# Kernel tuning notes

Measured on AMD Instinct MI355X. Metric: run time of the kernel, lower is better.

Reference implementation:

```python
import jax, jax.numpy as jnp
import numpy as np

B, C, T, H, W = 16, 3, 16, 224, 224
COLOR_STRENGTH = 0.3
NOISE_STRENGTH = 0.02
DROPOUT_PROB = 0.05
HFLIP_PROB = 0.5
MAX_JITTER = 3


def setup_inputs() -> dict:
    key = jax.random.key(0)
    ks = jax.random.split(key, 7)
    return {
        "video": jax.random.uniform(ks[0], (B, C, T, H, W), dtype=jnp.float32),
        "jitter": jax.random.randint(ks[1], (B,), 0, 2 * MAX_JITTER + 1, dtype=jnp.int32),
        "b_rand": jax.random.uniform(ks[2], (B,), dtype=jnp.float32),
        "c_rand": jax.random.uniform(ks[3], (B,), dtype=jnp.float32),
        "noise": jax.random.normal(ks[4], (B, C, T, H, W), dtype=jnp.float32),
        "flip_rand": jax.random.uniform(ks[5], (B,), dtype=jnp.float32),
        "drop_rand": jax.random.uniform(ks[6], (B, T), dtype=jnp.float32),
    }


def reference(video, jitter, b_rand, c_rand, noise, flip_rand, drop_rand):
    # --- GPUTemporalJitter: per-sample roll along T by j in [-MAX_JITTER, MAX_JITTER]
    j = jitter - MAX_JITTER                         # [B] in [-3, 3]
    t_idx = (jnp.arange(T)[None, :] - j[:, None]) % T  # roll semantics: out[t] = in[t - j]
    x = jnp.take_along_axis(video, t_idx[:, None, :, None, None], axis=2)

    # --- GPURandomBrightness: per-sample multiplicative factor, clamp [0,1]
    bf = 1.0 + (b_rand - 0.5) * 2.0 * COLOR_STRENGTH   # [B]
    x = jnp.clip(x * bf[:, None, None, None, None], 0.0, 1.0)

    # --- GPURandomContrast: (x-0.5)*c + 0.5 with c clamped to [0.1, 3.0], then clamp [0,1]
    cf = jnp.clip(1.0 + (c_rand - 0.5) * 2.0 * COLOR_STRENGTH, 0.1, 3.0)
    x = jnp.clip((x - 0.5) * cf[:, None, None, None, None] + 0.5, 0.0, 1.0)

    # --- GPURandomNoise: add gaussian noise, clamp [0,1]
    x = jnp.clip(x + noise * NOISE_STRENGTH, 0.0, 1.0)

    # --- GPURandomHorizontalFlip: per-sample flip along W
    flip_mask = flip_rand < HFLIP_PROB                 # [B]
    x = jnp.where(flip_mask[:, None, None, None, None], x[..., ::-1], x)

    # --- GPURandomFrameDropout: zero out frames, guarantee >=1 kept frame per sample
    keep = drop_rand > DROPOUT_PROB                    # [B, T]
    keep = keep.at[:, 0].set(keep[:, 0] | ~keep.any(axis=1))
    x = x * keep[:, None, :, None, None].astype(x.dtype)
    return x
```

## Files before the change

kernel.cpp:

```cpp
#include <hip/hip_runtime.h>

constexpr int Bn = 16, Cn = 3, Tn = 16, Hn = 224, Wn = 224;
constexpr int PLANE = Hn * Wn;
constexpr int THREADS = 256;
constexpr int FLOATS_PER_BLOCK = THREADS * 4;
constexpr int BLOCKS_PER_PLANE = PLANE / FLOATS_PER_BLOCK;

constexpr float COLOR_STRENGTH = 0.3f;
constexpr float NOISE_STRENGTH = 0.02f;
constexpr float DROPOUT_PROB   = 0.05f;
constexpr float HFLIP_PROB     = 0.5f;
constexpr int   MAX_JITTER     = 3;

__global__ __launch_bounds__(THREADS) void aug_kernel(
    const float* __restrict__ video,
    const int*   __restrict__ jitter,
    const float* __restrict__ b_rand,
    const float* __restrict__ c_rand,
    const float* __restrict__ noise,
    const float* __restrict__ flip_rand,
    const float* __restrict__ drop_rand,
    float*       __restrict__ out)
{
    const int bct = blockIdx.y;
    const int t = bct & (Tn - 1);
    const int c = (bct >> 4) % Cn;
    const int b = bct / (Tn * Cn);

    const int j = jitter[b] - MAX_JITTER;
    const int t_src = (t - j + Tn) & (Tn - 1);

    const float bf = 1.0f + (b_rand[b] - 0.5f) * (2.0f * COLOR_STRENGTH);
    float cf = 1.0f + (c_rand[b] - 0.5f) * (2.0f * COLOR_STRENGTH);
    cf = fminf(fmaxf(cf, 0.1f), 3.0f);

    const bool flip = flip_rand[b] < HFLIP_PROB;

    bool any_keep = false;
    #pragma unroll
    for (int tt = 0; tt < Tn; ++tt)
        any_keep = any_keep || (drop_rand[b * Tn + tt] > DROPOUT_PROB);
    bool keep = drop_rand[b * Tn + t] > DROPOUT_PROB;
    if (t == 0) keep = keep || !any_keep;
    const float keepf = keep ? 1.0f : 0.0f;

    const int inPlane  = ((b * Cn + c) * Tn + t_src) * PLANE;
    const int outPlane = ((b * Cn + c) * Tn + t) * PLANE;

    const int o = (blockIdx.x * THREADS + threadIdx.x) * 4;
    const int h = o / Wn;
    const int w = o - h * Wn;

    float4 v, nz;
    if (!flip) {
        v  = *(const float4*)(video + inPlane  + o);
        nz = *(const float4*)(noise + outPlane + o);
    } else {
        const int ws = Wn - 4 - w;
        const float4 vr = *(const float4*)(video + inPlane  + h * Wn + ws);
        const float4 nr = *(const float4*)(noise + outPlane + h * Wn + ws);
        v  = make_float4(vr.w, vr.z, vr.y, vr.x);
        nz = make_float4(nr.w, nr.z, nr.y, nr.x);
    }

    auto apply = [&](float x, float n) -> float {
        x = fminf(fmaxf(x * bf, 0.0f), 1.0f);
        x = fminf(fmaxf((x - 0.5f) * cf + 0.5f, 0.0f), 1.0f);
        x = fminf(fmaxf(x + n * NOISE_STRENGTH, 0.0f), 1.0f);
        return x * keepf;
    };

    float4 r;
    r.x = apply(v.x, nz.x);
    r.y = apply(v.y, nz.y);
    r.z = apply(v.z, nz.z);
    r.w = apply(v.w, nz.w);

    *(float4*)(out + outPlane + o) = r;
}

extern "C" void kernel_launch(void* const* d_in, const int* in_sizes, int n_in,
                              void* d_out, int out_size, void* d_ws, size_t ws_size,
                              hipStream_t stream) {
    const float* video     = (const float*)d_in[0];
    const int*   jitter    = (const int*)  d_in[1];
    const float* b_rand    = (const float*)d_in[2];
    const float* c_rand    = (const float*)d_in[3];
    const float* noise     = (const float*)d_in[4];
    const float* flip_rand = (const float*)d_in[5];
    const float* drop_rand = (const float*)d_in[6];
    float*       out       = (float*)d_out;

    dim3 grid(BLOCKS_PER_PLANE, Bn * Cn * Tn);
    aug_kernel<<<grid, dim3(THREADS), 0, stream>>>(
        video, jitter, b_rand, c_rand, noise, flip_rand, drop_rand, out);
}
```

Before: 352.5 us.

## Process seven float4s per thread with nontemporal loads and flip-on-store

Each thread now handles seven float4 elements, so the grid has seven times fewer blocks and every thread has more loads in flight. All loads and stores use nontemporal builtins to avoid polluting the cache on streaming data. The horizontal flip moves from the load side to the store side, so reads stay contiguous and only the write addresses are mirrored. This costs more registers per thread and fewer blocks, which could reduce occupancy or wave balance.

```diff
diff --git a/kernel.cpp b/kernel.cpp
--- a/kernel.cpp
+++ b/kernel.cpp
@@ -2,15 +2,19 @@
 
 constexpr int Bn = 16, Cn = 3, Tn = 16, Hn = 224, Wn = 224;
 constexpr int PLANE = Hn * Wn;
+constexpr int F4_PER_PLANE = PLANE / 4;
 constexpr int THREADS = 256;
-constexpr int FLOATS_PER_BLOCK = THREADS * 4;
-constexpr int BLOCKS_PER_PLANE = PLANE / FLOATS_PER_BLOCK;
+constexpr int PER_THREAD = 7;
+constexpr int BLOCKS_PER_PLANE = F4_PER_PLANE / (THREADS * PER_THREAD);
+constexpr int W4 = Wn / 4;
 
 constexpr float COLOR_STRENGTH = 0.3f;
 constexpr float NOISE_STRENGTH = 0.02f;
 constexpr float DROPOUT_PROB   = 0.05f;
 constexpr float HFLIP_PROB     = 0.5f;
 constexpr int   MAX_JITTER     = 3;
+
+typedef float v4f __attribute__((ext_vector_type(4)));
 
 __global__ __launch_bounds__(THREADS) void aug_kernel(
     const float* __restrict__ video,
@@ -44,23 +48,21 @@
     if (t == 0) keep = keep || !any_keep;
     const float keepf = keep ? 1.0f : 0.0f;
 
-    const int inPlane  = ((b * Cn + c) * Tn + t_src) * PLANE;
-    const int outPlane = ((b * Cn + c) * Tn + t) * PLANE;
+    const int inPlane4  = (((b * Cn + c) * Tn + t_src)) * F4_PER_PLANE;
+    const int outPlane4 = (((b * Cn + c) * Tn + t))     * F4_PER_PLANE;
 
-    const int o = (blockIdx.x * THREADS + threadIdx.x) * 4;
-    const int h = o / Wn;
-    const int w = o - h * Wn;
+    const v4f* __restrict__ vid4 = (const v4f*)video;
+    const v4f* __restrict__ noi4 = (const v4f*)noise;
+    v4f*       __restrict__ out4 = (v4f*)out;
 
-    float4 v, nz;
-    if (!flip) {
-        v  = *(const float4*)(video + inPlane  + o);
-        nz = *(const float4*)(noise + outPlane + o);
-    } else {
-        const int ws = Wn - 4 - w;
-        const float4 vr = *(const float4*)(video + inPlane  + h * Wn + ws);
-        const float4 nr = *(const float4*)(noise + outPlane + h * Wn + ws);
-        v  = make_float4(vr.w, vr.z, vr.y, vr.x);
-        nz = make_float4(nr.w, nr.z, nr.y, nr.x);
+    const int base = blockIdx.x * (PER_THREAD * THREADS) + threadIdx.x;
+
+    v4f v[PER_THREAD], nz[PER_THREAD];
+    #pragma unroll
+    for (int k = 0; k < PER_THREAD; ++k) {
+        const int p = base + k * THREADS;
+        v[k]  = __builtin_nontemporal_load(vid4 + inPlane4  + p);
+        nz[k] = __builtin_nontemporal_load(noi4 + outPlane4 + p);
     }
 
     auto apply = [&](float x, float n) -> float {
@@ -70,13 +72,25 @@
         return x * keepf;
     };
 
-    float4 r;
-    r.x = apply(v.x, nz.x);
-    r.y = apply(v.y, nz.y);
-    r.z = apply(v.z, nz.z);
-    r.w = apply(v.w, nz.w);
+    #pragma unroll
+    for (int k = 0; k < PER_THREAD; ++k) {
+        const int p = base + k * THREADS;
+        v4f r;
+        r.x = apply(v[k].x, nz[k].x);
+        r.y = apply(v[k].y, nz[k].y);
+        r.z = apply(v[k].z, nz[k].z);
+        r.w = apply(v[k].w, nz[k].w);
 
-    *(float4*)(out + outPlane + o) = r;
+        if (!flip) {
+            __builtin_nontemporal_store(r, out4 + outPlane4 + p);
+        } else {
+            const int row  = p / W4;
+            const int col  = p - row * W4;
+            const int pd   = row * W4 + (W4 - 1 - col);
+            v4f rr = { r.w, r.z, r.y, r.x };
+            __builtin_nontemporal_store(rr, out4 + outPlane4 + pd);
+        }
+    }
 }
 
 extern "C" void kernel_launch(void* const* d_in, const int* in_sizes, int n_in,
```

After: 339.9 us. 3.6% less time.
